# Performance work log

Measured on AMD Instinct MI355X. Metric: run time of the kernel, lower is better.

Reference implementation:

```python
import jax, jax.numpy as jnp
import numpy as np

N, D, K = 500_000, 64, 512


def setup_inputs() -> dict:
    key = jax.random.key(0)
    kx, kc = jax.random.split(key)
    x = jax.random.normal(kx, (N, D), dtype=jnp.float32)
    centroids = jax.random.normal(kc, (K, D), dtype=jnp.float32)
    return {"x": x, "centroids": centroids}


def reference(x, centroids):
    x2 = jnp.sum(x * x, axis=1, keepdims=True)            # [N, 1]
    c2 = jnp.sum(centroids * centroids, axis=1)           # [K]
    d2 = x2 + c2[None, :] - 2.0 * jnp.einsum('nd,kd->nk', x, centroids)
    d2 = jnp.maximum(d2, 0.0)
    # sqrt is monotonic so argmin over d2 == argmin over cdist
    label = jnp.argmin(d2, axis=1)                        # [N] int
    return label
```

## Files before the change

kernel.cpp:

```cpp
#include <hip/hip_runtime.h>

#define DIM 64
#define KC 512
#define BLK 256
#define BLKP 256
#define RSB 256
#define PT 2
#define CG 32
#define NT (CG / 16)
#define NGRP (KC / CG)
#define NTILE (KC / 16)
#define LIST_CAP 500000

#define MARGINH 2.0e-3f
#define SCALE_LO 4.8828125e-4f

typedef _Float16 half8   __attribute__((ext_vector_type(8)));
typedef float    floatx4 __attribute__((ext_vector_type(4)));

__device__ __forceinline__ void async_cp16(_Float16* lds_base, const _Float16* g_lane) {
    __builtin_amdgcn_global_load_lds(
        (const __attribute__((address_space(1))) unsigned int*)(g_lane),
        (__attribute__((address_space(3))) unsigned int*)(lds_base),
        16, 0, 0);
}

__global__ __launch_bounds__(BLKP) void kmeans_prep(
    const float* __restrict__ c, _Float16* __restrict__ frH,
    _Float16* __restrict__ frL, float* __restrict__ g_sc2,
    float* __restrict__ g_negh, unsigned* __restrict__ rs_count)
{
    const int b = blockIdx.x;
    if (b < 128) {
        const int e  = b * BLKP + threadIdx.x;
        const int cr = e >> 6, d = e & 63;
        const int T  = cr >> 4, ni = cr & 15;
        const int ch = d >> 5, q = (d >> 3) & 3, j = d & 7;
        const int pos = ((T * 2 + ch) * 64 + (q * 16 + ni)) * 8 + j;
        const float f = c[e];
        const _Float16 h = (_Float16)f;
        frH[pos] = h;
        frL[pos] = (_Float16)((f - (float)h) * 2048.0f);
    } else {
        if (b == 128 && threadIdx.x == 0) *rs_count = 0u;
        const int k = (b - 128) * BLKP + threadIdx.x;
        const float* crow = c + (long)k * DIM;
        float s0 = 0.f, s1 = 0.f, s2 = 0.f, s3 = 0.f;
        #pragma unroll
        for (int d = 0; d < DIM; d += 4) {
            s0 = fmaf(crow[d + 0], crow[d + 0], s0);
            s1 = fmaf(crow[d + 1], crow[d + 1], s1);
            s2 = fmaf(crow[d + 2], crow[d + 2], s2);
            s3 = fmaf(crow[d + 3], crow[d + 3], s3);
        }
        const float s = (s0 + s1) + (s2 + s3);
        g_sc2[k]  = s;
        g_negh[k] = -0.5f * s;
    }
}

__global__ __launch_bounds__(BLK)
__attribute__((amdgpu_waves_per_eu(2)))
void kmeans_mfma(const float* __restrict__ x,
                 const _Float16* __restrict__ frH, const _Float16* __restrict__ frL,
                 const float* __restrict__ g_negh, int* __restrict__ out,
                 unsigned* __restrict__ rs_count, int* __restrict__ rs_list, int n)
{
    __shared__ _Float16 shH[2][NT * 2 * 64 * 8];
    __shared__ _Float16 shL[2][NT * 2 * 64 * 8];
    __shared__ float    s_negh[KC];

    const int tid  = threadIdx.x;
    const int wave = tid >> 6;
    const int lane = tid & 63;
    const int nidx = lane & 15;
    const int quad = lane >> 4;

    const long jobBase = ((long)blockIdx.x * 4 + wave) * (PT * 16);

    auto stage = [&](int gg, int buf) {
        const _Float16* srcH = frH + (long)gg * (NT * 2 * 64 * 8);
        const _Float16* srcL = frL + (long)gg * (NT * 2 * 64 * 8);
        const int chunk = wave * 64;
        async_cp16(&shH[buf][(long)chunk * 8], srcH + (long)(chunk + lane) * 8);
        async_cp16(&shL[buf][(long)chunk * 8], srcL + (long)(chunk + lane) * 8);
    };

    stage(0, 0);
    for (int k2 = tid; k2 < KC; k2 += BLK) s_negh[k2] = g_negh[k2];

    half8 ah[PT][2], al[PT][2];
    #pragma unroll
    for (int pt = 0; pt < PT; ++pt) {
        long row = jobBase + pt * 16 + nidx;
        if (row > (long)n - 1) row = (long)n - 1;
        #pragma unroll
        for (int ch = 0; ch < 2; ++ch) {
            const float* xp = x + row * DIM + ch * 32 + quad * 8;
            float4 v0 = *(const float4*)xp;
            float4 v1 = *(const float4*)(xp + 4);
            float fs[8] = {v0.x, v0.y, v0.z, v0.w, v1.x, v1.y, v1.z, v1.w};
            #pragma unroll
            for (int j = 0; j < 8; ++j) {
                _Float16 h = (_Float16)fs[j];
                ah[pt][ch][j] = h;
                al[pt][ch][j] = (_Float16)((fs[j] - (float)h) * 2048.0f);
            }
        }
    }

    float best[PT][4], sec[PT][4];
    #pragma unroll
    for (int pt = 0; pt < PT; ++pt)
        #pragma unroll
        for (int r = 0; r < 4; ++r) {
            best[pt][r] = -3.402823466e38f;
            sec[pt][r]  = -3.402823466e38f;
        }

    const floatx4 ZERO = {0.f, 0.f, 0.f, 0.f};

    __syncthreads();

    for (int g = 0; g < NGRP; ++g) {
        const int cur = g & 1;
        if (g + 1 < NGRP) stage(g + 1, cur ^ 1);

        #pragma unroll
        for (int t = 0; t < NT; ++t) {
            const half8 bh0 = *(const half8*)&shH[cur][((t * 2 + 0) * 64 + lane) * 8];
            const half8 bh1 = *(const half8*)&shH[cur][((t * 2 + 1) * 64 + lane) * 8];
            const half8 bl0 = *(const half8*)&shL[cur][((t * 2 + 0) * 64 + lane) * 8];
            const half8 bl1 = *(const half8*)&shL[cur][((t * 2 + 1) * 64 + lane) * 8];
            const int   T5    = g * NT + t;
            const float ng    = s_negh[T5 * 16 + nidx];
            const floatx4 cinit = {ng, ng, ng, ng};
            #pragma unroll
            for (int pt = 0; pt < PT; ++pt) {
                floatx4 am, ac;
                am = __builtin_amdgcn_mfma_f32_16x16x32_f16(ah[pt][0], bh0, cinit, 0, 0, 0);
                am = __builtin_amdgcn_mfma_f32_16x16x32_f16(ah[pt][1], bh1, am, 0, 0, 0);
                ac = __builtin_amdgcn_mfma_f32_16x16x32_f16(ah[pt][0], bl0, ZERO, 0, 0, 0);
                ac = __builtin_amdgcn_mfma_f32_16x16x32_f16(ah[pt][1], bl1, ac, 0, 0, 0);
                ac = __builtin_amdgcn_mfma_f32_16x16x32_f16(al[pt][0], bh0, ac, 0, 0, 0);
                ac = __builtin_amdgcn_mfma_f32_16x16x32_f16(al[pt][1], bh1, ac, 0, 0, 0);
                #pragma unroll
                for (int r = 0; r < 4; ++r) {
                    const float vv = fmaf(ac[r], SCALE_LO, am[r]);
                    const float vp = __uint_as_float(
                        (__float_as_uint(vv) & 0xFFFFFFE0u) | (unsigned)T5);
                    sec[pt][r]  = __builtin_amdgcn_fmed3f(sec[pt][r], vp, best[pt][r]);
                    best[pt][r] = fmaxf(best[pt][r], vp);
                }
            }
        }
        if (g + 1 < NGRP) __syncthreads();
    }

    int bidx[PT][4];
    #pragma unroll
    for (int pt = 0; pt < PT; ++pt)
        #pragma unroll
        for (int r = 0; r < 4; ++r)
            bidx[pt][r] = (int)((__float_as_uint(best[pt][r]) & 31u) << 4) + nidx;

    #pragma unroll
    for (int off = 1; off < 16; off <<= 1) {
        #pragma unroll
        for (int pt = 0; pt < PT; ++pt)
            #pragma unroll
            for (int r = 0; r < 4; ++r) {
                const float ob = __shfl_xor(best[pt][r], off, 64);
                const int   oi = __shfl_xor(bidx[pt][r], off, 64);
                const float os = __shfl_xor(sec[pt][r],  off, 64);
                const bool take = (ob > best[pt][r]) ||
                                  (ob == best[pt][r] && oi < bidx[pt][r]);
                const float loser = take ? best[pt][r] : ob;
                sec[pt][r]  = fmaxf(fmaxf(sec[pt][r], os), loser);
                best[pt][r] = take ? ob : best[pt][r];
                bidx[pt][r] = take ? oi : bidx[pt][r];
            }
    }

    const int pt_w = nidx >> 2;
    const int r_w  = nidx & 3;
    float b = 0.f, s = 0.f; int bi = 0;
    #pragma unroll
    for (int pt = 0; pt < PT; ++pt)
        #pragma unroll
        for (int r = 0; r < 4; ++r) {
            const bool m = (pt == pt_w) && (r == r_w);
            b  = m ? best[pt][r] : b;
            s  = m ? sec[pt][r]  : s;
            bi = m ? bidx[pt][r] : bi;
        }
    const long p = jobBase + (long)pt_w * 16 + quad * 4 + r_w;

    const bool valid = (nidx < 8) && (p < n);
    if (valid) out[p] = bi;
    const bool need  = valid && !(b - s > MARGINH);

    const unsigned long long m = __ballot(need);
    if (m) {
        const int leader = (int)(__ffsll((unsigned long long)m) - 1);
        unsigned base = 0;
        if (lane == leader) base = atomicAdd(rs_count, (unsigned)__popcll(m));
        base = __shfl(base, leader, 64);
        if (need) {
            const unsigned idx = base + (unsigned)__popcll(m & ((1ull << lane) - 1ull));
            if (idx < LIST_CAP) rs_list[idx] = (int)p;
        }
    }
}

__global__ __launch_bounds__(RSB) void kmeans_rescan(
    const float* __restrict__ x, const float* __restrict__ c,
    const float* __restrict__ g_sc2, const unsigned* __restrict__ rs_count,
    const int* __restrict__ rs_list, int* __restrict__ out)
{
    __shared__ float4 ct4[16 * 513];
    __shared__ float  s_c2[KC];

    unsigned cnt = *rs_count;
    if (cnt > LIST_CAP) cnt = LIST_CAP;
    if ((unsigned)(blockIdx.x * (RSB / 64)) >= cnt) return;

    const int tid = threadIdx.x;
    for (int e = tid; e < KC * 16; e += RSB) {
        const int k = e >> 4, d4 = e & 15;
        ct4[d4 * 513 + k] = *(const float4*)(c + (long)k * DIM + d4 * 4);
    }
    for (int k = tid; k < KC; k += RSB) s_c2[k] = g_sc2[k];
    __syncthreads();

    const int lane  = tid & 63;
    const int gwave = blockIdx.x * (RSB / 64) + (tid >> 6);
    const int nwave = gridDim.x * (RSB / 64);

    for (unsigned j = gwave; j < cnt; j += nwave) {
        const int p = rs_list[j];
        const float* xrow = x + (long)p * DIM;

        float x20 = 0.f, x21 = 0.f, x22 = 0.f, x23 = 0.f;
        #pragma unroll
        for (int d = 0; d < DIM; d += 4) {
            x20 = fmaf(xrow[d + 0], xrow[d + 0], x20);
            x21 = fmaf(xrow[d + 1], xrow[d + 1], x21);
            x22 = fmaf(xrow[d + 2], xrow[d + 2], x22);
            x23 = fmaf(xrow[d + 3], xrow[d + 3], x23);
        }
        const float x2 = (x20 + x21) + (x22 + x23);

        float bb = 3.402823466e38f; int bbi = 0x7fffffff;
        #pragma unroll
        for (int kk = 0; kk < 8; ++kk) {
            const int k = kk * 64 + lane;
            float d0 = 0.f, d1 = 0.f, d2a = 0.f, d3 = 0.f;
            #pragma unroll
            for (int d4 = 0; d4 < 16; ++d4) {
                const float4 q = ct4[d4 * 513 + k];
                d0  = fmaf(q.x, xrow[4 * d4 + 0], d0);
                d1  = fmaf(q.y, xrow[4 * d4 + 1], d1);
                d2a = fmaf(q.z, xrow[4 * d4 + 2], d2a);
                d3  = fmaf(q.w, xrow[4 * d4 + 3], d3);
            }
            const float dot = (d0 + d1) + (d2a + d3);
            float d2v = (x2 + s_c2[k]) - 2.0f * dot;
            d2v = fmaxf(d2v, 0.0f);
            const bool l2 = (d2v < bb) || (d2v == bb && k < bbi);
            bb  = l2 ? d2v : bb;
            bbi = l2 ? k   : bbi;
        }
        #pragma unroll
        for (int off = 1; off < 64; off <<= 1) {
            const float ob = __shfl_xor(bb, off, 64);
            const int   oi = __shfl_xor(bbi, off, 64);
            const bool take = (ob < bb) || (ob == bb && oi < bbi);
            bb  = take ? ob : bb;
            bbi = take ? oi : bbi;
        }
        if (lane == 0) out[p] = bbi;
    }
}

extern "C" void kernel_launch(void* const* d_in, const int* in_sizes, int n_in,
                              void* d_out, int out_size, void* d_ws, size_t ws_size,
                              hipStream_t stream) {
    const float* x = (const float*)d_in[0];
    const float* c = (const float*)d_in[1];
    int* out = (int*)d_out;
    const int n = in_sizes[0] / DIM;

    _Float16* frH   = (_Float16*)d_ws;
    _Float16* frL   = frH + (KC * DIM);
    float*    gsc2  = (float*)(frL + (KC * DIM));
    float*    gnegh = gsc2 + KC;
    unsigned* cnt   = (unsigned*)(gnegh + KC);
    int*      rlist = (int*)(cnt + 4);

    kmeans_prep<<<130, BLKP, 0, stream>>>(c, frH, frL, gsc2, gnegh, cnt);

    const int jobs   = (n + PT * 16 - 1) / (PT * 16);
    const int blocks = (jobs + 3) / 4;
    kmeans_mfma<<<blocks, BLK, 0, stream>>>(x, frH, frL, gnegh, out, cnt, rlist, n);

    kmeans_rescan<<<256, RSB, 0, stream>>>(x, c, gsc2, cnt, rlist, out);
}
```

Before: 300.3 us.

## Fuse prep, MFMA argmin and rescan into one kernel with in-block centroid conversion

Merges the three kernels into one. Each block computes centroid norms, converts centroids to the split fp16 hi/lo layout in registers, and writes them to LDS, which replaces the async global-to-LDS copy of precomputed fragments. Rows with a narrow best/second margin are re-scanned exactly inside the same wave from global centroids, so the atomic list and the separate rescan launch go away. This removes two launches and the workspace round trip. In exchange every block redoes the centroid norm and conversion work, and the inline rescan reads centroids from global or cache in a serial per-row loop inside the main kernel.

```diff
diff --git a/kernel.cpp b/kernel.cpp
--- a/kernel.cpp
+++ b/kernel.cpp
@@ -3,14 +3,10 @@
 #define DIM 64
 #define KC 512
 #define BLK 256
-#define BLKP 256
-#define RSB 256
 #define PT 2
 #define CG 32
 #define NT (CG / 16)
 #define NGRP (KC / CG)
-#define NTILE (KC / 16)
-#define LIST_CAP 500000
 
 #define MARGINH 2.0e-3f
 #define SCALE_LO 4.8828125e-4f
@@ -18,32 +14,27 @@
 typedef _Float16 half8   __attribute__((ext_vector_type(8)));
 typedef float    floatx4 __attribute__((ext_vector_type(4)));
 
-__device__ __forceinline__ void async_cp16(_Float16* lds_base, const _Float16* g_lane) {
-    __builtin_amdgcn_global_load_lds(
-        (const __attribute__((address_space(1))) unsigned int*)(g_lane),
-        (__attribute__((address_space(3))) unsigned int*)(lds_base),
-        16, 0, 0);
-}
-
-__global__ __launch_bounds__(BLKP) void kmeans_prep(
-    const float* __restrict__ c, _Float16* __restrict__ frH,
-    _Float16* __restrict__ frL, float* __restrict__ g_sc2,
-    float* __restrict__ g_negh, unsigned* __restrict__ rs_count)
+__global__ __launch_bounds__(BLK)
+__attribute__((amdgpu_waves_per_eu(2)))
+void kmeans_fused(const float* __restrict__ x, const float* __restrict__ c,
+                  int* __restrict__ out, int n)
 {
-    const int b = blockIdx.x;
-    if (b < 128) {
-        const int e  = b * BLKP + threadIdx.x;
-        const int cr = e >> 6, d = e & 63;
-        const int T  = cr >> 4, ni = cr & 15;
-        const int ch = d >> 5, q = (d >> 3) & 3, j = d & 7;
-        const int pos = ((T * 2 + ch) * 64 + (q * 16 + ni)) * 8 + j;
-        const float f = c[e];
-        const _Float16 h = (_Float16)f;
-        frH[pos] = h;
-        frL[pos] = (_Float16)((f - (float)h) * 2048.0f);
-    } else {
-        if (b == 128 && threadIdx.x == 0) *rs_count = 0u;
-        const int k = (b - 128) * BLKP + threadIdx.x;
+    __shared__ _Float16 shH[2][NT * 2 * 64 * 8];
+    __shared__ _Float16 shL[2][NT * 2 * 64 * 8];
+    __shared__ float    s_negh[KC];
+    __shared__ float    s_sc2[KC];
+
+    const int tid  = threadIdx.x;
+    const int wave = tid >> 6;
+    const int lane = tid & 63;
+    const int nidx = lane & 15;
+    const int quad = lane >> 4;
+
+    const long jobBase = ((long)blockIdx.x * 4 + wave) * (PT * 16);
+
+    #pragma unroll
+    for (int kk = 0; kk < 2; ++kk) {
+        const int k = kk * BLK + tid;
         const float* crow = c + (long)k * DIM;
         float s0 = 0.f, s1 = 0.f, s2 = 0.f, s3 = 0.f;
         #pragma unroll
@@ -54,40 +45,35 @@
             s3 = fmaf(crow[d + 3], crow[d + 3], s3);
         }
         const float s = (s0 + s1) + (s2 + s3);
-        g_sc2[k]  = s;
-        g_negh[k] = -0.5f * s;
-    }
-}
-
-__global__ __launch_bounds__(BLK)
-__attribute__((amdgpu_waves_per_eu(2)))
-void kmeans_mfma(const float* __restrict__ x,
-                 const _Float16* __restrict__ frH, const _Float16* __restrict__ frL,
-                 const float* __restrict__ g_negh, int* __restrict__ out,
-                 unsigned* __restrict__ rs_count, int* __restrict__ rs_list, int n)
-{
-    __shared__ _Float16 shH[2][NT * 2 * 64 * 8];
-    __shared__ _Float16 shL[2][NT * 2 * 64 * 8];
-    __shared__ float    s_negh[KC];
-
-    const int tid  = threadIdx.x;
-    const int wave = tid >> 6;
-    const int lane = tid & 63;
-    const int nidx = lane & 15;
-    const int quad = lane >> 4;
-
-    const long jobBase = ((long)blockIdx.x * 4 + wave) * (PT * 16);
-
-    auto stage = [&](int gg, int buf) {
-        const _Float16* srcH = frH + (long)gg * (NT * 2 * 64 * 8);
-        const _Float16* srcL = frL + (long)gg * (NT * 2 * 64 * 8);
-        const int chunk = wave * 64;
-        async_cp16(&shH[buf][(long)chunk * 8], srcH + (long)(chunk + lane) * 8);
-        async_cp16(&shL[buf][(long)chunk * 8], srcL + (long)(chunk + lane) * 8);
+        s_sc2[k]  = s;
+        s_negh[k] = -0.5f * s;
+    }
+
+    const int m_tt = (tid >> 7) & 1;
+    const int m_ch = (tid >> 6) & 1;
+    const int m_q  = (tid >> 4) & 3;
+    const int m_ni = tid & 15;
+    const int crd  = (m_tt * 16 + m_ni) * DIM + m_ch * 32 + m_q * 8;
+
+    auto cvt_store = [&](int buf, const float4& v0, const float4& v1) {
+        const float fs[8] = {v0.x, v0.y, v0.z, v0.w, v1.x, v1.y, v1.z, v1.w};
+        half8 hh, ll;
+        #pragma unroll
+        for (int j = 0; j < 8; ++j) {
+            const _Float16 h = (_Float16)fs[j];
+            hh[j] = h;
+            ll[j] = (_Float16)((fs[j] - (float)h) * 2048.0f);
+        }
+        *(half8*)&shH[buf][tid * 8] = hh;
+        *(half8*)&shL[buf][tid * 8] = ll;
     };
 
-    stage(0, 0);
-    for (int k2 = tid; k2 < KC; k2 += BLK) s_negh[k2] = g_negh[k2];
+    {
+        const float* src = c + crd;
+        const float4 v0 = *(const float4*)src;
+        const float4 v1 = *(const float4*)(src + 4);
+        cvt_store(0, v0, v1);
+    }
 
     half8 ah[PT][2], al[PT][2];
     #pragma unroll
@@ -124,7 +110,12 @@
 
     for (int g = 0; g < NGRP; ++g) {
         const int cur = g & 1;
-        if (g + 1 < NGRP) stage(g + 1, cur ^ 1);
+        float4 nv0, nv1;
+        if (g + 1 < NGRP) {
+            const float* src = c + (long)(g + 1) * CG * DIM + crd;
+            nv0 = *(const float4*)src;
+            nv1 = *(const float4*)(src + 4);
+        }
 
         #pragma unroll
         for (int t = 0; t < NT; ++t) {
@@ -154,7 +145,11 @@
                 }
             }
         }
-        if (g + 1 < NGRP) __syncthreads();
+
+        if (g + 1 < NGRP) {
+            cvt_store(cur ^ 1, nv0, nv1);
+            __syncthreads();
+        }
     }
 
     int bidx[PT][4];
@@ -200,47 +195,13 @@
     if (valid) out[p] = bi;
     const bool need  = valid && !(b - s > MARGINH);
 
-    const unsigned long long m = __ballot(need);
-    if (m) {
-        const int leader = (int)(__ffsll((unsigned long long)m) - 1);
-        unsigned base = 0;
-        if (lane == leader) base = atomicAdd(rs_count, (unsigned)__popcll(m));
-        base = __shfl(base, leader, 64);
-        if (need) {
-            const unsigned idx = base + (unsigned)__popcll(m & ((1ull << lane) - 1ull));
-            if (idx < LIST_CAP) rs_list[idx] = (int)p;
-        }
-    }
-}
-
-__global__ __launch_bounds__(RSB) void kmeans_rescan(
-    const float* __restrict__ x, const float* __restrict__ c,
-    const float* __restrict__ g_sc2, const unsigned* __restrict__ rs_count,
-    const int* __restrict__ rs_list, int* __restrict__ out)
-{
-    __shared__ float4 ct4[16 * 513];
-    __shared__ float  s_c2[KC];
-
-    unsigned cnt = *rs_count;
-    if (cnt > LIST_CAP) cnt = LIST_CAP;
-    if ((unsigned)(blockIdx.x * (RSB / 64)) >= cnt) return;
-
-    const int tid = threadIdx.x;
-    for (int e = tid; e < KC * 16; e += RSB) {
-        const int k = e >> 4, d4 = e & 15;
-        ct4[d4 * 513 + k] = *(const float4*)(c + (long)k * DIM + d4 * 4);
-    }
-    for (int k = tid; k < KC; k += RSB) s_c2[k] = g_sc2[k];
-    __syncthreads();
-
-    const int lane  = tid & 63;
-    const int gwave = blockIdx.x * (RSB / 64) + (tid >> 6);
-    const int nwave = gridDim.x * (RSB / 64);
-
-    for (unsigned j = gwave; j < cnt; j += nwave) {
-        const int p = rs_list[j];
-        const float* xrow = x + (long)p * DIM;
-
+    unsigned long long mm = __ballot(need);
+    while (mm) {
+        const int ol = (int)(__ffsll(mm) - 1);
+        mm &= (mm - 1ull);
+        const int pp = __builtin_amdgcn_readfirstlane(__shfl((int)p, ol, 64));
+
+        const float* xrow = x + (long)pp * DIM;
         float x20 = 0.f, x21 = 0.f, x22 = 0.f, x23 = 0.f;
         #pragma unroll
         for (int d = 0; d < DIM; d += 4) {
@@ -253,19 +214,20 @@
 
         float bb = 3.402823466e38f; int bbi = 0x7fffffff;
         #pragma unroll
-        for (int kk = 0; kk < 8; ++kk) {
-            const int k = kk * 64 + lane;
+        for (int kk2 = 0; kk2 < 8; ++kk2) {
+            const int k = kk2 * 64 + lane;
+            const float* crow = c + (long)k * DIM;
             float d0 = 0.f, d1 = 0.f, d2a = 0.f, d3 = 0.f;
             #pragma unroll
             for (int d4 = 0; d4 < 16; ++d4) {
-                const float4 q = ct4[d4 * 513 + k];
-                d0  = fmaf(q.x, xrow[4 * d4 + 0], d0);
-                d1  = fmaf(q.y, xrow[4 * d4 + 1], d1);
-                d2a = fmaf(q.z, xrow[4 * d4 + 2], d2a);
-                d3  = fmaf(q.w, xrow[4 * d4 + 3], d3);
+                const float4 q4 = *(const float4*)(crow + d4 * 4);
+                d0  = fmaf(q4.x, xrow[4 * d4 + 0], d0);
+                d1  = fmaf(q4.y, xrow[4 * d4 + 1], d1);
+                d2a = fmaf(q4.z, xrow[4 * d4 + 2], d2a);
+                d3  = fmaf(q4.w, xrow[4 * d4 + 3], d3);
             }
             const float dot = (d0 + d1) + (d2a + d3);
-            float d2v = (x2 + s_c2[k]) - 2.0f * dot;
+            float d2v = (x2 + s_sc2[k]) - 2.0f * dot;
             d2v = fmaxf(d2v, 0.0f);
             const bool l2 = (d2v < bb) || (d2v == bb && k < bbi);
             bb  = l2 ? d2v : bb;
@@ -279,7 +241,7 @@
             bb  = take ? ob : bb;
             bbi = take ? oi : bbi;
         }
-        if (lane == 0) out[p] = bbi;
+        if (lane == 0) out[pp] = bbi;
     }
 }
 
@@ -291,18 +253,9 @@
     int* out = (int*)d_out;
     const int n = in_sizes[0] / DIM;
 
-    _Float16* frH   = (_Float16*)d_ws;
-    _Float16* frL   = frH + (KC * DIM);
-    float*    gsc2  = (float*)(frL + (KC * DIM));
-    float*    gnegh = gsc2 + KC;
-    unsigned* cnt   = (unsigned*)(gnegh + KC);
-    int*      rlist = (int*)(cnt + 4);
-
-    kmeans_prep<<<130, BLKP, 0, stream>>>(c, frH, frL, gsc2, gnegh, cnt);
+    (void)d_ws; (void)ws_size;
 
     const int jobs   = (n + PT * 16 - 1) / (PT * 16);
     const int blocks = (jobs + 3) / 4;
-    kmeans_mfma<<<blocks, BLK, 0, stream>>>(x, frH, frL, gnegh, out, cnt, rlist, n);
-
-    kmeans_rescan<<<256, RSB, 0, stream>>>(x, c, gsc2, cnt, rlist, out);
+    kmeans_fused<<<blocks, BLK, 0, stream>>>(x, c, out, n);
 }
```

After: 454.5 us. +51.4%, slower.
